# Kernel tuning notes

Hardware: AMD Instinct MI355X
Metric: run time of the kernel (lower is better)

## Reference

```python
import jax, jax.numpy as jnp
import numpy as np
from jax import lax

NEG = -1e30  # log-space 'zero' that stays finite for stable grads

T, B, V, L = 2000, 64, 128, 100


def ctc_cost(acts, labels2d, sizes, label_lens):
    """warp-ctc style CTC: acts are raw logits (T,B,V), blank index 0.
    Returns summed negative log-likelihood over the batch, shape (1,)."""
    Tn, Bn, Vn = acts.shape
    Ln = labels2d.shape[1]
    S = 2 * Ln + 1  # extended label length: blank,l1,blank,l2,...,blank
    lp = jax.nn.log_softmax(acts, axis=-1)  # (T,B,V)

    # extended label sequence per example: even positions blank(0), odd = labels
    ext = jnp.zeros((Bn, S), dtype=labels2d.dtype).at[:, 1::2].set(labels2d)
    # skip (s-2 -> s) allowed iff ext[s] != blank and ext[s] != ext[s-2]
    prev2 = jnp.concatenate([jnp.full((Bn, 2), -1, ext.dtype), ext[:, :-2]], axis=1)
    can_skip = (ext != 0) & (ext != prev2)  # (B,S)

    # gather per-state emission log-probs for all timesteps: (T,B,S)
    lp_ext = jnp.take_along_axis(lp, jnp.broadcast_to(ext[None], (Tn, Bn, S)), axis=2)

    # alpha init at t=0: states 0 (blank) and 1 (first label)
    alpha0 = (jnp.full((Bn, S), NEG, lp.dtype)
              .at[:, 0].set(lp_ext[0, :, 0])
              .at[:, 1].set(lp_ext[0, :, 1]))

    # per-timestep activity mask: freeze alpha once t >= sizes[b]
    active = jnp.arange(1, Tn)[:, None] < sizes[None, :]  # (T-1, B)

    def step(alpha, x):
        lp_t, act = x  # (B,S), (B,)
        a1 = jnp.concatenate([jnp.full((Bn, 1), NEG, alpha.dtype), alpha[:, :-1]], axis=1)
        a2 = jnp.concatenate([jnp.full((Bn, 2), NEG, alpha.dtype), alpha[:, :-2]], axis=1)
        a2 = jnp.where(can_skip, a2, NEG)
        new = jnp.logaddexp(jnp.logaddexp(alpha, a1), a2) + lp_t
        alpha = jnp.where(act[:, None], new, alpha)
        return alpha, None

    alpha, _ = lax.scan(step, alpha0, (lp_ext[1:], active))

    # log-likelihood ends at extended states S_b-1 (final blank) and S_b-2 (final label)
    S_b = 2 * label_lens + 1
    last = jnp.take_along_axis(alpha, (S_b - 1)[:, None], axis=1)[:, 0]
    last2 = jnp.take_along_axis(alpha, (S_b - 2)[:, None], axis=1)[:, 0]
    ll = jnp.logaddexp(last, last2)  # (B,)
    return -jnp.sum(ll)[None]  # shape (1,) like the torch module


def setup_inputs() -> dict:
    key = jax.random.key(0)
    k1, k2, k3 = jax.random.split(key, 3)
    inp = jax.random.normal(k1, (T, B, V), dtype=jnp.float32)
    # labels in [1, V): 0 is reserved for blank
    target = jax.random.randint(k2, (B * L,), 1, V, dtype=jnp.int32)
    # frame counts in [T//2, T], always >= 2L+1 so every path is feasible
    sizes = jax.random.randint(k3, (B,), T // 2, T + 1, dtype=jnp.int32)
    label_lens = jnp.full((B,), L, dtype=jnp.int32)
    return {"input": inp, "target": target, "sizes": sizes, "label_lens": label_lens}


def reference(input, target, sizes, label_lens):
    labels2d = target.reshape(sizes.shape[0], -1)  # all label_lens equal -> clean reshape
    return ctc_cost(input, labels2d, sizes, label_lens)
```

## Files before the change

### kernel.cpp

```cpp
#include <hip/hip_runtime.h>


#define TT 2000
#define BB 64
#define VV 128
#define LL 100
#define REC 104
#define REC_BASE 256
#define NEGF (-1e30f)
#define L2E 1.44269504f
#define LN2 0.69314718f

#define SLOTW 1088
#define NSLOT 4
#define EXCH_BASE (NSLOT * SLOTW)
#define WREG (NSLOT * SLOTW + 384)
#define SB_STATE (REC_BASE + BB * TT * REC)
#define AREA 336

__device__ __forceinline__ float wave_max64(float v) {
#pragma unroll
  for (int o = 32; o > 0; o >>= 1) v = fmaxf(v, __shfl_xor(v, o, 64));
  return v;
}
__device__ __forceinline__ float wave_sum64(float v) {
#pragma unroll
  for (int o = 32; o > 0; o >>= 1) v += __shfl_xor(v, o, 64);
  return v;
}

__global__ __launch_bounds__(256) void k_gather(const float* __restrict__ acts,
                                                const int* __restrict__ target,
                                                float* __restrict__ ws) {
  const int lane = threadIdx.x & 63;
  const int w = threadIdx.x >> 6;
  const int r = blockIdx.x * 4 + w;
  if (r >= TT * BB) return;
  const int b = r % BB;
  const int t = r / BB;
  const float* row = acts + (size_t)r * VV;
  float x0 = row[lane];
  float x1 = row[lane + 64];
  float m = wave_max64(fmaxf(x0, x1));
  float e = __builtin_exp2f((x0 - m) * L2E) + __builtin_exp2f((x1 - m) * L2E);
  float s = wave_sum64(e);
  float lse = m + __builtin_log2f(s) * LN2;
  const int* lab = target + b * LL;
  int c1 = lab[lane];
  int j2 = 64 + lane;
  int c2 = (j2 < LL) ? lab[j2] : 1;
  float y1lo = __shfl(x0, c1 & 63, 64);
  float y1hi = __shfl(x1, c1 & 63, 64);
  float y1 = (c1 < 64) ? y1lo : y1hi;
  float y2lo = __shfl(x0, c2 & 63, 64);
  float y2hi = __shfl(x1, c2 & 63, 64);
  float y2 = (c2 < 64) ? y2lo : y2hi;
  float g1 = y1 - lse;
  float g2 = (j2 < LL) ? (y2 - lse) : NEGF;
  float gb = __shfl(x0, 0, 64) - lse;
  float gm = wave_max64(fmaxf(fmaxf(g1, g2), gb));
  float q1 = __builtin_exp2f((g1 - gm) * L2E);
  float q2 = (j2 < LL) ? __builtin_exp2f((g2 - gm) * L2E) : 0.0f;
  float* rec = ws + REC_BASE + ((size_t)b * TT + t) * REC;
  rec[2 + lane] = q1;
  if (lane < 38) rec[66 + lane] = q2;
  if (lane == 0) { rec[0] = __builtin_exp2f((gb - gm) * L2E); rec[1] = gm; }
}

__device__ __forceinline__ void gl_lds16(const float* g, float* l) {
  __builtin_amdgcn_global_load_lds(
      (const __attribute__((address_space(1))) unsigned int*)g,
      (__attribute__((address_space(3))) unsigned int*)l, 16, 0, 0);
}
__device__ __forceinline__ void gl_lds4(const float* g, float* l) {
  __builtin_amdgcn_global_load_lds(
      (const __attribute__((address_space(1))) unsigned int*)g,
      (__attribute__((address_space(3))) unsigned int*)l, 4, 0, 0);
}
#define WAITV(N) do { asm volatile("s_waitcnt vmcnt(" #N ")" ::: "memory");  \
                      __builtin_amdgcn_sched_barrier(0); } while (0)
#define BPER __builtin_amdgcn_ds_bpermute

#define ISSUE(bidx) do {                                                     \
  int bi_ = (bidx); bi_ = (bi_ < bcap) ? bi_ : bcap; if (bi_ < 0) bi_ = 0;   \
  float* sb_ = lds + (((unsigned)(bidx)) & 3u) * SLOTW;                      \
  const float* r0_ = recs_b + (size_t)(tA + TS * 4 * bi_) * REC;             \
  const float* q_ = r0_ + qbase;                                             \
  gl_lds16(q_,                 sb_);                                         \
  gl_lds16(q_ + TS * REC,      sb_ + 256);                                   \
  gl_lds16(q_ + TS * 2 * REC,  sb_ + 512);                                   \
  gl_lds16(q_ + TS * 3 * REC,  sb_ + 768);                                   \
  gl_lds4(r0_ + hoff,          sb_ + 1024);                                  \
} while (0)

#define DECLR(P) float4 P##q0, P##q1, P##q2, P##q3, P##h01, P##h23; float P##aY

#define LOADR(P, bidx) do {                                                  \
  const float* sb_ = lds + (((unsigned)(bidx)) & 3u) * SLOTW;                \
  float4 V0_ = *(const float4*)(sb_ + 4 * l);                                \
  float4 V1_ = *(const float4*)(sb_ + 256 + 4 * l);                          \
  float4 V2_ = *(const float4*)(sb_ + 512 + 4 * l);                          \
  float4 V3_ = *(const float4*)(sb_ + 768 + 4 * l);                          \
  if constexpr (DIR) {                                                       \
    P##q0 = (float4){V0_.w, V0_.z, V0_.y * cmask, V0_.x * cmask};            \
    P##q1 = (float4){V1_.w, V1_.z, V1_.y * cmask, V1_.x * cmask};            \
    P##q2 = (float4){V2_.w, V2_.z, V2_.y * cmask, V2_.x * cmask};            \
    P##q3 = (float4){V3_.w, V3_.z, V3_.y * cmask, V3_.x * cmask};            \
  } else { P##q0 = V0_; P##q1 = V1_; P##q2 = V2_; P##q3 = V3_; }             \
  P##h01 = *(const float4*)(sb_ + 1024);                                     \
  P##h23 = *(const float4*)(sb_ + 1028);                                     \
  P##aY = sb_[aoff];                                                         \
} while (0)

#define STEP(qbv, gmv, cx, cy, bx, by, ay, NH) do {                          \
  const float qb_ = (qbv); msum += (gmv);                                    \
  o3 = __builtin_fmaf(cs_o3, o1, o3 + o2) * (cy);                            \
  o2 = (o2 + o1) * qb_;                                                      \
  o1 = __builtin_fmaf(cs_o1, h1, o1 + o0) * (cx);                            \
  o0 = (o0 + h1) * qb_;                                                      \
  if (NH >= 1) { h1 = __builtin_fmaf(cs_h1, h3, h1 + h2) * (by);             \
                 h2 = (h2 + h3) * qb_; }                                     \
  if (NH >= 2) { h3 = __builtin_fmaf(cs_h3, h5, h3 + h4) * (bx);             \
                 h4 = (h4 + h5) * qb_; }                                     \
  if (NH >= 3) { h5 = __builtin_fmaf(cs_h5, h7, h5 + h6) * (ay);             \
                 h6 = (h6 + h7) * qb_; }                                     \
} while (0)

#define COMPA(P) do {                                                        \
  STEP(P##h01.x, P##h01.y, P##q0.z, P##q0.w, P##q0.x, P##q0.y, P##aY, 3);    \
  STEP(P##h01.z, P##h01.w, P##q1.z, P##q1.w, P##q1.x, P##q1.y, 0.f, 2);      \
  STEP(P##h23.x, P##h23.y, P##q2.z, P##q2.w, P##q2.x, P##q2.y, 0.f, 1);      \
  STEP(P##h23.z, P##h23.w, P##q3.z, P##q3.w, 0.f, 0.f, 0.f, 0);              \
  *(float4*)(exb + 4 * l) = (float4){o0, o1, o2, o3};                        \
  ((int*)exb)[256 + l] = offs;                                               \
} while (0)

#define FINL() do {                                                          \
  asm volatile("" ::: "memory");   \
  float4 L1_ = *(const float4*)(exb + 4 * ((l >= 1) ? (l - 1) : 0));         \
  float4 L2_ = *(const float4*)(exb + 4 * ((l >= 2) ? (l - 2) : 0));         \
  int ro1_ = ((const int*)exb)[256 + ((l >= 1) ? (l - 1) : 0)];              \
  int ro2_ = ((const int*)exb)[256 + ((l >= 2) ? (l - 2) : 0)];              \
  ro1_ = (l >= 1) ? ro1_ : -(1 << 29);                                       \
  ro2_ = (l >= 2) ? ro2_ : -(1 << 29);                                       \
  float m_ = fmaxf(fmaxf(o0, o1), fmaxf(o2, o3));                            \
  int eb_ = (int)((__float_as_uint(m_) >> 23) & 255u);                       \
  int t1_ = offs + (eb_ ? (eb_ - 127) : -126);                               \
  int mx_ = (ro1_ > ro2_) ? ro1_ : ro2_;                                     \
  int onew_ = (t1_ > mx_) ? t1_ : mx_;                                       \
  int ds_ = offs - onew_;  ds_ = (ds_ < -300) ? -300 : ds_;                  \
  int d1_ = ro1_ - onew_, d2_ = ro2_ - onew_;                                \
  d1_ = (d1_ < -300) ? -300 : d1_;                                           \
  d2_ = (d2_ < -300) ? -300 : d2_;                                           \
  o0 = ldexpf(o0, ds_); o1 = ldexpf(o1, ds_);                                \
  o2 = ldexpf(o2, ds_); o3 = ldexpf(o3, ds_);                                \
  h1 = ldexpf(L1_.w, d1_) * msk1;                                            \
  h2 = ldexpf(L1_.z, d1_) * msk2;                                            \
  h3 = ldexpf(L1_.y, d1_) * msk3;                                            \
  h4 = ldexpf(L1_.x, d1_) * msk4;                                            \
  h5 = ldexpf(L2_.w, d2_) * msk5;                                            \
  h6 = ldexpf(L2_.z, d2_) * msk6;                                            \
  h7 = ldexpf(L2_.y, d2_) * msk7;                                            \
  offs = onew_;                                                              \
} while (0)

template <int DIR>
__device__ __forceinline__ void run_chain(const int* __restrict__ target,
                                          const int* __restrict__ lablens,
                                          const float* __restrict__ recs_b,
                                          float* lds, int size, int b, int l,
                                          float* __restrict__ ws) {
  float* exb = lds + EXCH_BASE;
  const int mid = (size - 1) >> 1;
  const int sizeP = DIR ? (size - 1 - mid) : (mid + 1);
  const int* lab = target + b * LL;
  const int lc = (l < 50) ? l : 50;
  const int qbase = DIR ? (100 - 2 * lc) : (2 * lc);
  const int tA = DIR ? (size - 2) : 1;
  constexpr int TS = DIR ? -1 : 1;
  const int bcap = DIR ? ((size - 5) >> 2) : 498;
  const int hoff = (l < 8) ? (TS * (l >> 1) * REC + (l & 1)) : 0;
  const int aoff = (l >= 1) ? (4 * (l - 1) + (DIR ? 2 : 1)) : 0;
  const float cmask = (l < 50) ? 1.f : 0.f;
  const int idx1 = ((l + 63) & 63) << 2;
  const float msk1 = (4 * l - 1 >= 0) ? 1.f : 0.f;
  const float msk2 = (4 * l - 2 >= 0) ? 1.f : 0.f;
  const float msk3 = (4 * l - 3 >= 0) ? 1.f : 0.f;
  const float msk4 = (4 * l - 4 >= 0) ? 1.f : 0.f;
  const float msk5 = (4 * l - 5 >= 0) ? 1.f : 0.f;
  const float msk6 = (4 * l - 6 >= 0) ? 1.f : 0.f;
  const float msk7 = (4 * l - 7 >= 0) ? 1.f : 0.f;
  int i0, i1, i2, i3, i4, i5;
  if constexpr (DIR == 0) { i0 = 2*l+1; i1 = 2*l; i2 = 2*l-1; i3 = 2*l-2; i4 = 2*l-3; i5 = 2*l-4; }
  else { i0 = 98-2*l; i1 = 99-2*l; i2 = 100-2*l; i3 = 101-2*l; i4 = 102-2*l; i5 = 103-2*l; }
#define CLM(x) ((x) < 0 ? 0 : ((x) > 99 ? 99 : (x)))
  const int La = lab[CLM(i0)], Lb_ = lab[CLM(i1)], Lc = lab[CLM(i2)];
  const int Ld = lab[CLM(i3)], Le = lab[CLM(i4)], Lf = lab[CLM(i5)];
  const float cs_o3 = (La != Lb_) ? 1.f : 0.f;
  const float cs_o1 = (Lb_ != Lc) ? 1.f : 0.f;
  const float cs_h1 = (Lc != Ld) ? 1.f : 0.f;
  const float cs_h3 = (Ld != Le) ? 1.f : 0.f;
  const float cs_h5 = (Le != Lf) ? 1.f : 0.f;
  float o0 = 0.f, o1 = 0.f, o2 = 0.f, o3 = 0.f;
  float h1 = 0.f, h2 = 0.f, h3 = 0.f, h4 = 0.f, h5 = 0.f, h6 = 0.f, h7 = 0.f;
  int offs = 0;
  float msum;
  if constexpr (DIR == 0) {
    msum = recs_b[1];
    if (l == 0) { o0 = recs_b[0]; o1 = recs_b[2]; }
    if (l == 1) { h3 = recs_b[2]; h4 = recs_b[0]; }
    if (l == 2) { h7 = recs_b[2]; }
  } else {
    const float* recL = recs_b + (size_t)(size - 1) * REC;
    msum = recL[1];
    const int Lbv = lablens[b];
    const int r0v = 200 - 2 * Lbv;
    auto gi = [&](int rho) -> float {
      if (rho != r0v && rho != r0v + 1) return 0.f;
      if ((rho & 1) == 0) return recL[0];
      return recL[2 + 99 - ((rho - 1) >> 1)];
    };
    o0 = gi(4*l); o1 = gi(4*l+1); o2 = gi(4*l+2); o3 = gi(4*l+3);
    h1 = gi(4*l-1); h2 = gi(4*l-2); h3 = gi(4*l-3); h4 = gi(4*l-4);
    h5 = gi(4*l-5); h6 = gi(4*l-6); h7 = gi(4*l-7);
  }

  const int nb = (sizeP - 1) >> 2;
  DECLR(A); DECLR(B);
  ISSUE(0); ISSUE(1); ISSUE(2);
  WAITV(10);
  LOADR(A, 0);
  int blk = 0;
  for (; blk + 2 <= nb; blk += 2) {
    COMPA(A); ISSUE(blk + 3); WAITV(10); LOADR(B, blk + 1); FINL();
    COMPA(B); ISSUE(blk + 4); WAITV(10); LOADR(A, blk + 2); FINL();
  }
  WAITV(0);
  if (blk < nb) { COMPA(A); FINL(); }
  {
    int rno1 = BPER(idx1, offs);
    int dtl = rno1 - offs;
    dtl = (dtl > 120) ? 120 : ((dtl < -300) ? -300 : dtl);
    for (int tau = 1 + 4 * nb; tau < sizeP; ++tau) {
      const float* rt = recs_b + (size_t)(DIR ? (size - 1 - tau) : tau) * REC;
      float2 hh = *(const float2*)rt;
      float cx, cy;
      if constexpr (DIR == 0) {
        float2 qc = *(const float2*)(rt + 2 + 2 * lc);
        cx = qc.x; cy = qc.y;
      } else {
        float2 qc = *(const float2*)(rt + qbase);
        cx = qc.y * cmask; cy = qc.x * cmask;
      }
      int rp = BPER(idx1, __float_as_int(o3));
      float p = ldexpf(__int_as_float(rp), dtl) * msk1;
      msum += hh.y;
      o3 = __builtin_fmaf(cs_o3, o1, o3 + o2) * cy;
      o2 = (o2 + o1) * hh.x;
      o1 = __builtin_fmaf(cs_o1, p, o1 + o0) * cx;
      o0 = (o0 + p) * hh.x;
    }
    if constexpr (DIR == 0) {
      int rp = BPER(idx1, __float_as_int(o3));
      float p = ldexpf(__int_as_float(rp), dtl) * msk1;
      o3 = __builtin_fmaf(cs_o3, o1, o3 + o2);
      o2 = o2 + o1;
      o1 = __builtin_fmaf(cs_o1, p, o1 + o0);
      o0 = o0 + p;
    }
  }
  float* da = ws + SB_STATE + (size_t)(2 * b + DIR) * AREA;
  ((float4*)da)[l] = (float4){o0, o1, o2, o3};
  ((int*)da)[256 + l] = offs;
  if (l == 0) da[320] = msum;
}

__global__ __launch_bounds__(128, 1) void k_alpha(const int* __restrict__ target,
                                                  const int* __restrict__ sizes,
                                                  const int* __restrict__ lablens,
                                                  float* __restrict__ ws) {
  __shared__ float ldsA[2 * WREG];
  const int b = blockIdx.x;
  const int dirw = threadIdx.x >> 6;
  const int l = threadIdx.x & 63;
  float* lds = ldsA + dirw * WREG;
  const int size = sizes[b];
  const float* recs_b = ws + REC_BASE + (size_t)b * TT * REC;
  if (dirw == 0) run_chain<0>(target, lablens, recs_b, lds, size, b, l, ws);
  else           run_chain<1>(target, lablens, recs_b, lds, size, b, l, ws);
}

__global__ __launch_bounds__(64) void k_comb(float* __restrict__ ws) {
  const int b = blockIdx.x;
  const int l = threadIdx.x;
  const float* fa = ws + SB_STATE + (size_t)(2 * b) * AREA;
  const float* ba = fa + AREA;
  float4 av = ((const float4*)fa)[l];
  int eF = ((const int*)fa)[256 + l];
  float msF = fa[320], msB = ba[320];
  float pr0, pr1, pr2, pr3; int ex0, ex1, ex2, ex3, sb0, sb1, sb2, sb3;
#define CMP(k, AV, PR, EX, SBE) do {                                         \
    int s_ = 4 * l + (k);                                                    \
    int rho_ = 200 - s_;                                                     \
    int rc_ = (rho_ < 0) ? 0 : rho_;                                         \
    float g_ = ba[rc_];                                                      \
    int eB_ = ((const int*)ba)[256 + (rc_ >> 2)];                            \
    float p_ = (AV) * g_;                                                    \
    bool ok_ = (rho_ >= 0) && (p_ > 0.f);                                    \
    int eb_ = (int)((__float_as_uint(p_) >> 23) & 255u);                     \
    SBE = eF + eB_;                                                          \
    EX = ok_ ? (SBE + (eb_ ? eb_ - 127 : -140)) : (int)0xC0000000;           \
    PR = ok_ ? p_ : 0.f;                                                     \
  } while (0)
  CMP(0, av.x, pr0, ex0, sb0);
  CMP(1, av.y, pr1, ex1, sb1);
  CMP(2, av.z, pr2, ex2, sb2);
  CMP(3, av.w, pr3, ex3, sb3);
  int Em = ex0 > ex1 ? ex0 : ex1;
  Em = ex2 > Em ? ex2 : Em;
  Em = ex3 > Em ? ex3 : Em;
#pragma unroll
  for (int o = 32; o > 0; o >>= 1) {
    int t = __shfl_xor(Em, o, 64);
    Em = (t > Em) ? t : Em;
  }
  float v = 0.f;
#define ACC(PR, SBE) do { if (PR > 0.f) {                                    \
    int sh_ = SBE - Em; sh_ = sh_ < -300 ? -300 : (sh_ > 300 ? 300 : sh_);   \
    v += ldexpf(PR, sh_); } } while (0)
  ACC(pr0, sb0); ACC(pr1, sb1); ACC(pr2, sb2); ACC(pr3, sb3);
  float S = wave_sum64(v);
  if (l == 0) ws[b] = msF + msB + LN2 * ((float)Em + __builtin_log2f(S));
}

__global__ __launch_bounds__(64) void k_final(const float* __restrict__ ws, float* __restrict__ out) {
  float v = (threadIdx.x < BB) ? ws[threadIdx.x] : 0.0f;
  v = wave_sum64(v);
  if (threadIdx.x == 0) out[0] = -v;
}

extern "C" void kernel_launch(void* const* d_in, const int* in_sizes, int n_in,
                              void* d_out, int out_size, void* d_ws, size_t ws_size,
                              hipStream_t stream) {
  const float* acts  = (const float*)d_in[0];
  const int* target  = (const int*)d_in[1];
  const int* sizes   = (const int*)d_in[2];
  const int* lablens = (const int*)d_in[3];
  float* ws  = (float*)d_ws;
  float* out = (float*)d_out;
  const int nrec = TT * BB;
  k_gather<<<dim3(nrec / 4), dim3(256), 0, stream>>>(acts, target, ws);
  k_alpha<<<dim3(BB), dim3(128), 0, stream>>>(target, sizes, lablens, ws);
  k_comb<<<dim3(BB), dim3(64), 0, stream>>>(ws);
  k_final<<<dim3(1), dim3(64), 0, stream>>>(ws, out);
}
```

Measured before the change: 145.4 us.

## Replace LDS-staged async prefetch with direct register prefetch, four-deep rotation

The alpha/beta chain kernel used to stage each 4-step block of emission records through a 4-slot LDS ring using global_load_lds, with explicit vmcnt waits. It now loads each lane's records straight from global memory into registers, keeping four register buffers in rotation so loads for three blocks ahead are in flight. This removes the LDS round trip and the manual waitcnt and sched barriers, and shrinks LDS use to just the exchange buffer. In exchange it uses more VGPRs and relies on the compiler's waitcnt placement to overlap latency, which could stall the serial recurrence if the compiler waits too early.

```diff
diff --git a/kernel.cpp b/kernel.cpp
--- a/kernel.cpp
+++ b/kernel.cpp
@@ -11,10 +11,6 @@
 #define L2E 1.44269504f
 #define LN2 0.69314718f
 
-#define SLOTW 1088
-#define NSLOT 4
-#define EXCH_BASE (NSLOT * SLOTW)
-#define WREG (NSLOT * SLOTW + 384)
 #define SB_STATE (REC_BASE + BB * TT * REC)
 #define AREA 336
 
@@ -67,49 +63,38 @@
   if (lane == 0) { rec[0] = __builtin_exp2f((gb - gm) * L2E); rec[1] = gm; }
 }
 
-__device__ __forceinline__ void gl_lds16(const float* g, float* l) {
-  __builtin_amdgcn_global_load_lds(
-      (const __attribute__((address_space(1))) unsigned int*)g,
-      (__attribute__((address_space(3))) unsigned int*)l, 16, 0, 0);
-}
-__device__ __forceinline__ void gl_lds4(const float* g, float* l) {
-  __builtin_amdgcn_global_load_lds(
-      (const __attribute__((address_space(1))) unsigned int*)g,
-      (__attribute__((address_space(3))) unsigned int*)l, 4, 0, 0);
-}
-#define WAITV(N) do { asm volatile("s_waitcnt vmcnt(" #N ")" ::: "memory");  \
-                      __builtin_amdgcn_sched_barrier(0); } while (0)
 #define BPER __builtin_amdgcn_ds_bpermute
 
-#define ISSUE(bidx) do {                                                     \
+#define DECLR(P) float2 P##h0, P##h1, P##h2, P##h3; \
+                 float4 P##q0, P##q1, P##q2, P##q3; float P##aY
+
+#define PREF(P, bidx) do {                                                   \
   int bi_ = (bidx); bi_ = (bi_ < bcap) ? bi_ : bcap; if (bi_ < 0) bi_ = 0;   \
-  float* sb_ = lds + (((unsigned)(bidx)) & 3u) * SLOTW;                      \
   const float* r0_ = recs_b + (size_t)(tA + TS * 4 * bi_) * REC;             \
-  const float* q_ = r0_ + qbase;                                             \
-  gl_lds16(q_,                 sb_);                                         \
-  gl_lds16(q_ + TS * REC,      sb_ + 256);                                   \
-  gl_lds16(q_ + TS * 2 * REC,  sb_ + 512);                                   \
-  gl_lds16(q_ + TS * 3 * REC,  sb_ + 768);                                   \
-  gl_lds4(r0_ + hoff,          sb_ + 1024);                                  \
-} while (0)
-
-#define DECLR(P) float4 P##q0, P##q1, P##q2, P##q3, P##h01, P##h23; float P##aY
-
-#define LOADR(P, bidx) do {                                                  \
-  const float* sb_ = lds + (((unsigned)(bidx)) & 3u) * SLOTW;                \
-  float4 V0_ = *(const float4*)(sb_ + 4 * l);                                \
-  float4 V1_ = *(const float4*)(sb_ + 256 + 4 * l);                          \
-  float4 V2_ = *(const float4*)(sb_ + 512 + 4 * l);                          \
-  float4 V3_ = *(const float4*)(sb_ + 768 + 4 * l);                          \
+  P##h0 = *(const float2*)(r0_);                                             \
+  P##h1 = *(const float2*)(r0_ + TS * REC);                                  \
+  P##h2 = *(const float2*)(r0_ + TS * 2 * REC);                              \
+  P##h3 = *(const float2*)(r0_ + TS * 3 * REC);                              \
+  float2 lo0_ = *(const float2*)(r0_ + vofs);                                \
+  float2 hi0_ = *(const float2*)(r0_ + vofs + 2);                            \
+  float2 lo1_ = *(const float2*)(r0_ + TS * REC + vofs);                     \
+  float2 hi1_ = *(const float2*)(r0_ + TS * REC + vofs + 2);                 \
+  float2 lo2_ = *(const float2*)(r0_ + TS * 2 * REC + vofs);                 \
+  float2 hi2_ = *(const float2*)(r0_ + TS * 2 * REC + vofs + 2);             \
+  float2 lo3_ = *(const float2*)(r0_ + TS * 3 * REC + vofs);                 \
+  float2 hi3_ = *(const float2*)(r0_ + TS * 3 * REC + vofs + 2);             \
+  P##aY = r0_[ayofs];                                                        \
   if constexpr (DIR) {                                                       \
-    P##q0 = (float4){V0_.w, V0_.z, V0_.y * cmask, V0_.x * cmask};            \
-    P##q1 = (float4){V1_.w, V1_.z, V1_.y * cmask, V1_.x * cmask};            \
-    P##q2 = (float4){V2_.w, V2_.z, V2_.y * cmask, V2_.x * cmask};            \
-    P##q3 = (float4){V3_.w, V3_.z, V3_.y * cmask, V3_.x * cmask};            \
-  } else { P##q0 = V0_; P##q1 = V1_; P##q2 = V2_; P##q3 = V3_; }             \
-  P##h01 = *(const float4*)(sb_ + 1024);                                     \
-  P##h23 = *(const float4*)(sb_ + 1028);                                     \
-  P##aY = sb_[aoff];                                                         \
+    P##q0 = (float4){hi0_.y, hi0_.x, lo0_.y * cmask, lo0_.x * cmask};        \
+    P##q1 = (float4){hi1_.y, hi1_.x, lo1_.y * cmask, lo1_.x * cmask};        \
+    P##q2 = (float4){hi2_.y, hi2_.x, lo2_.y * cmask, lo2_.x * cmask};        \
+    P##q3 = (float4){hi3_.y, hi3_.x, lo3_.y * cmask, lo3_.x * cmask};        \
+  } else {                                                                   \
+    P##q0 = (float4){lo0_.x, lo0_.y, hi0_.x, hi0_.y};                        \
+    P##q1 = (float4){lo1_.x, lo1_.y, hi1_.x, hi1_.y};                        \
+    P##q2 = (float4){lo2_.x, lo2_.y, hi2_.x, hi2_.y};                        \
+    P##q3 = (float4){lo3_.x, lo3_.y, hi3_.x, hi3_.y};                        \
+  }                                                                          \
 } while (0)
 
 #define STEP(qbv, gmv, cx, cy, bx, by, ay, NH) do {                          \
@@ -127,16 +112,16 @@
 } while (0)
 
 #define COMPA(P) do {                                                        \
-  STEP(P##h01.x, P##h01.y, P##q0.z, P##q0.w, P##q0.x, P##q0.y, P##aY, 3);    \
-  STEP(P##h01.z, P##h01.w, P##q1.z, P##q1.w, P##q1.x, P##q1.y, 0.f, 2);      \
-  STEP(P##h23.x, P##h23.y, P##q2.z, P##q2.w, P##q2.x, P##q2.y, 0.f, 1);      \
-  STEP(P##h23.z, P##h23.w, P##q3.z, P##q3.w, 0.f, 0.f, 0.f, 0);              \
+  STEP(P##h0.x, P##h0.y, P##q0.z, P##q0.w, P##q0.x, P##q0.y, P##aY, 3);      \
+  STEP(P##h1.x, P##h1.y, P##q1.z, P##q1.w, P##q1.x, P##q1.y, 0.f, 2);        \
+  STEP(P##h2.x, P##h2.y, P##q2.z, P##q2.w, P##q2.x, P##q2.y, 0.f, 1);        \
+  STEP(P##h3.x, P##h3.y, P##q3.z, P##q3.w, 0.f, 0.f, 0.f, 0);                \
   *(float4*)(exb + 4 * l) = (float4){o0, o1, o2, o3};                        \
   ((int*)exb)[256 + l] = offs;                                               \
 } while (0)
 
 #define FINL() do {                                                          \
-  asm volatile("" ::: "memory");   \
+  asm volatile("" ::: "memory");                                             \
   float4 L1_ = *(const float4*)(exb + 4 * ((l >= 1) ? (l - 1) : 0));         \
   float4 L2_ = *(const float4*)(exb + 4 * ((l >= 2) ? (l - 2) : 0));         \
   int ro1_ = ((const int*)exb)[256 + ((l >= 1) ? (l - 1) : 0)];              \
@@ -168,19 +153,19 @@
 __device__ __forceinline__ void run_chain(const int* __restrict__ target,
                                           const int* __restrict__ lablens,
                                           const float* __restrict__ recs_b,
-                                          float* lds, int size, int b, int l,
+                                          float* exb, int size, int b, int l,
                                           float* __restrict__ ws) {
-  float* exb = lds + EXCH_BASE;
   const int mid = (size - 1) >> 1;
   const int sizeP = DIR ? (size - 1 - mid) : (mid + 1);
   const int* lab = target + b * LL;
   const int lc = (l < 50) ? l : 50;
-  const int qbase = DIR ? (100 - 2 * lc) : (2 * lc);
+  const int vofs = DIR ? (100 - 2 * lc) : (2 * lc);
   const int tA = DIR ? (size - 2) : 1;
   constexpr int TS = DIR ? -1 : 1;
   const int bcap = DIR ? ((size - 5) >> 2) : 498;
-  const int hoff = (l < 8) ? (TS * (l >> 1) * REC + (l & 1)) : 0;
-  const int aoff = (l >= 1) ? (4 * (l - 1) + (DIR ? 2 : 1)) : 0;
+  int ay_ = DIR ? (104 - 2 * l) : (2 * l - 1);
+  ay_ = (ay_ < 0) ? 0 : ((ay_ > 103) ? 103 : ay_);
+  const int ayofs = ay_;
   const float cmask = (l < 50) ? 1.f : 0.f;
   const int idx1 = ((l + 63) & 63) << 2;
   const float msk1 = (4 * l - 1 >= 0) ? 1.f : 0.f;
@@ -226,17 +211,18 @@
   }
 
   const int nb = (sizeP - 1) >> 2;
-  DECLR(A); DECLR(B);
-  ISSUE(0); ISSUE(1); ISSUE(2);
-  WAITV(10);
-  LOADR(A, 0);
+  DECLR(A); DECLR(B); DECLR(C); DECLR(D);
+  PREF(A, 0); PREF(B, 1); PREF(C, 2);
   int blk = 0;
-  for (; blk + 2 <= nb; blk += 2) {
-    COMPA(A); ISSUE(blk + 3); WAITV(10); LOADR(B, blk + 1); FINL();
-    COMPA(B); ISSUE(blk + 4); WAITV(10); LOADR(A, blk + 2); FINL();
+  for (; blk + 4 <= nb; blk += 4) {
+    COMPA(A); PREF(D, blk + 3); FINL();
+    COMPA(B); PREF(A, blk + 4); FINL();
+    COMPA(C); PREF(B, blk + 5); FINL();
+    COMPA(D); PREF(C, blk + 6); FINL();
   }
-  WAITV(0);
-  if (blk < nb) { COMPA(A); FINL(); }
+  if (nb - blk >= 1) { COMPA(A); FINL(); }
+  if (nb - blk >= 2) { COMPA(B); FINL(); }
+  if (nb - blk >= 3) { COMPA(C); FINL(); }
   {
     int rno1 = BPER(idx1, offs);
     int dtl = rno1 - offs;
@@ -249,7 +235,7 @@
         float2 qc = *(const float2*)(rt + 2 + 2 * lc);
         cx = qc.x; cy = qc.y;
       } else {
-        float2 qc = *(const float2*)(rt + qbase);
+        float2 qc = *(const float2*)(rt + vofs + 2);
         cx = qc.y * cmask; cy = qc.x * cmask;
       }
       int rp = BPER(idx1, __float_as_int(o3));
@@ -279,15 +265,15 @@
                                                   const int* __restrict__ sizes,
                                                   const int* __restrict__ lablens,
                                                   float* __restrict__ ws) {
-  __shared__ float ldsA[2 * WREG];
+  __shared__ float ldsA[2 * 384];
   const int b = blockIdx.x;
   const int dirw = threadIdx.x >> 6;
   const int l = threadIdx.x & 63;
-  float* lds = ldsA + dirw * WREG;
+  float* exb = ldsA + dirw * 384;
   const int size = sizes[b];
   const float* recs_b = ws + REC_BASE + (size_t)b * TT * REC;
-  if (dirw == 0) run_chain<0>(target, lablens, recs_b, lds, size, b, l, ws);
-  else           run_chain<1>(target, lablens, recs_b, lds, size, b, l, ws);
+  if (dirw == 0) run_chain<0>(target, lablens, recs_b, exb, size, b, l, ws);
+  else           run_chain<1>(target, lablens, recs_b, exb, size, b, l, ws);
 }
 
 __global__ __launch_bounds__(64) void k_comb(float* __restrict__ ws) {
```

Result: faster. 131.2 us (-9.8%).
